# Performance work log

Measured on AMD Instinct MI355X. Metric: run time of the kernel, lower is better.

## Reference

```python
import jax, jax.numpy as jnp
import numpy as np

B, H, V, MSG_MAX_LEN = 16384, 512, 32, 20


def setup_inputs() -> dict:
    key = jax.random.key(0)
    ks = jax.random.split(key, 8)
    s = 0.05  # weight scale so softmax stays well-conditioned
    return {
        "encoder_hidden": jax.random.normal(ks[0], (B, H), jnp.float32),
        "encoder_cell": jax.random.normal(ks[1], (B, H), jnp.float32),
        "W_ih": jax.random.normal(ks[2], (4 * H, V), jnp.float32) * s,
        "b_ih": jax.random.normal(ks[3], (4 * H,), jnp.float32) * s,
        "W_hh": jax.random.normal(ks[4], (4 * H, H), jnp.float32) * s,
        "b_hh": jax.random.normal(ks[5], (4 * H,), jnp.float32) * s,
        "W_out": jax.random.normal(ks[6], (V, H), jnp.float32) * s,
        "b_out": jax.random.normal(ks[7], (V,), jnp.float32) * s,
        "init_input": jnp.zeros((1, V), jnp.float32),
        "eos_idx": 31,
    }


def reference(encoder_hidden, encoder_cell, W_ih, b_ih, W_hh, b_hh, W_out, b_out, init_input, eos_idx):
    batch = encoder_hidden.shape[0]
    vocab = W_out.shape[0]
    # Original code never updates decoder_input (typo 'deocder_input'), so the
    # LSTM input is init_input every step -> input projection is loop-invariant.
    x = jnp.broadcast_to(init_input, (batch, init_input.shape[1]))
    x_proj = x @ W_ih.T + b_ih  # [B, 4H]

    def step(carry, _):
        h, c, mask, lp = carry  # h,c: [B,H]; mask: [1,B]; lp: scalar
        mask_out = mask  # mask is appended BEFORE the update in the original
        gates = x_proj + h @ W_hh.T + b_hh
        i, f, g, o = jnp.split(gates, 4, axis=1)  # torch LSTMCell gate order i,f,g,o
        i = jax.nn.sigmoid(i); f = jax.nn.sigmoid(f)
        g = jnp.tanh(g); o = jax.nn.sigmoid(o)
        c = f * c + i * g
        h = o * jnp.tanh(c)
        probs = jax.nn.softmax(h @ W_out.T + b_out, axis=1)  # [B,V]
        predict = jax.nn.one_hot(jnp.argmax(probs, axis=1), vocab, dtype=probs.dtype)  # eval-mode branch
        lp = lp + jnp.log((probs * predict).sum(axis=1)) @ mask[0]
        new_mask = mask * (1.0 - predict[:, eos_idx])  # zero out finished sequences
        return (h, c, new_mask, lp), (predict, mask_out)

    init = (encoder_hidden, encoder_cell,
            jnp.ones((1, batch), encoder_hidden.dtype),
            jnp.zeros((), encoder_hidden.dtype))
    (_, _, _, log_probs), (message, mask) = jax.lax.scan(step, init, None, length=MSG_MAX_LEN)
    return message, mask, log_probs  # [L,B,V], [L,1,B], scalar
```

## Files before the change

kernel.cpp:

```cpp
#include <hip/hip_runtime.h>
#include <math.h>

#define BATCH 16384
#define HDIM  512
#define VOCAB 32
#define STEPS 20
#define G4    2048

typedef _Float16 f16;
typedef _Float16 f16x8 __attribute__((ext_vector_type(8)));
typedef float    f32x16 __attribute__((ext_vector_type(16)));

#define SH   256.0f
#define SW   1024.0f
#define SINV (1.0f / (SH * SW))


__device__ __forceinline__ void gload16(const void* g, void* l) {
#if defined(__has_builtin) && __has_builtin(__builtin_amdgcn_global_load_lds)
    __builtin_amdgcn_global_load_lds(
        (const __attribute__((address_space(1))) void*)g,
        (__attribute__((address_space(3))) void*)l, 16, 0, 0);
#else
    *(float4*)l = *(const float4*)g;
#endif
}

__device__ __forceinline__ float fsig(float x)  { return 1.0f / (1.0f + __expf(-x)); }
__device__ __forceinline__ float ftanh(float x) { return 1.0f - 2.0f / (__expf(2.0f * x) + 1.0f); }

__global__ void init_xb_kernel(const float* __restrict__ W_ih,
                               const float* __restrict__ b_ih,
                               const float* __restrict__ b_hh,
                               const float* __restrict__ x0,
                               float* __restrict__ xb) {
    int n = blockIdx.x * blockDim.x + threadIdx.x;
    if (n >= G4) return;
    float s = b_ih[n] + b_hh[n];
    const float* wr = W_ih + (size_t)n * VOCAB;
    #pragma unroll
    for (int v = 0; v < VOCAB; v++) s += wr[v] * x0[v];
    xb[n] = s;
}

__global__ void init_mask_kernel(float* __restrict__ mask) {
    int b = blockIdx.x * blockDim.x + threadIdx.x;
    if (b < BATCH) mask[b] = 1.0f;
}

__global__ void wimg_kernel(const float* __restrict__ W_hh,
                            f16* __restrict__ Wh, f16* __restrict__ Wl) {
    size_t g  = (size_t)blockIdx.x * 256 + threadIdx.x;
    int ln = g & 63;  size_t r = g >> 6;
    int gg = r & 3;   size_t r2 = r >> 2;
    int ks = r2 & 1;  size_t r3 = r2 >> 1;
    int kc = r3 & 15; int jb = (int)(r3 >> 4);
    int n = gg * 512 + jb * 32 + (ln & 31);
    int k = kc * 32 + ks * 16 + (ln >> 5) * 8;
    const float* s = W_hh + (size_t)n * HDIM + k;
    f16x8 vh, vl;
    #pragma unroll
    for (int i = 0; i < 8; i++) {
        float x = s[i] * SW;
        f16 h = (f16)x;
        vh[i] = h;
        vl[i] = (f16)(x - (float)h);
    }
    *(f16x8*)(Wh + g * 8) = vh;
    *(f16x8*)(Wl + g * 8) = vl;
}

__global__ void woutimg_kernel(const float* __restrict__ W_out,
                               f16* __restrict__ Oh, f16* __restrict__ Ol) {
    int g  = blockIdx.x * 256 + threadIdx.x;
    int ln = g & 63;
    int r  = g >> 6;
    int kc = r >> 1, ks = r & 1;
    int v  = ln & 31;
    int k  = kc * 32 + ks * 16 + (ln >> 5) * 8;
    const float* s = W_out + (size_t)v * HDIM + k;
    f16x8 vh, vl;
    #pragma unroll
    for (int i = 0; i < 8; i++) {
        float x = s[i] * SW;
        f16 h = (f16)x;
        vh[i] = h;
        vl[i] = (f16)(x - (float)h);
    }
    *(f16x8*)(Oh + (size_t)g * 8) = vh;
    *(f16x8*)(Ol + (size_t)g * 8) = vl;
}

__global__ void hT_init_kernel(const float* __restrict__ src,
                               f16* __restrict__ dh, f16* __restrict__ dl) {
    size_t g = (size_t)blockIdx.x * 256 + threadIdx.x;
    int ln = g & 63;  size_t r = g >> 6;
    int mb = (int)(r & 511); int kk = (int)(r >> 9);
    int m = mb * 32 + (ln & 31);
    int k = kk * 16 + (ln >> 5) * 8;
    const float* s = src + (size_t)m * HDIM + k;
    f16x8 vh, vl;
    #pragma unroll
    for (int i = 0; i < 8; i++) {
        float x = s[i] * SH;
        f16 h = (f16)x;
        vh[i] = h;
        vl[i] = (f16)(x - (float)h);
    }
    *(f16x8*)(dh + g * 8) = vh;
    *(f16x8*)(dl + g * 8) = vl;
}

__device__ __forceinline__ void out_body(int lane, int mb,
        const f16* __restrict__ hTh, const f16* __restrict__ hTl,
        const f16* __restrict__ Oh,  const f16* __restrict__ Ol,
        const float* __restrict__ b_out,
        float* __restrict__ mask, float* __restrict__ msg_t,
        float* __restrict__ maskout_t, float* __restrict__ lp_part, int eos) {
    const int half = lane >> 5;
    const int l31  = lane & 31;

    f32x16 acc;
    #pragma unroll
    for (int r = 0; r < 16; r++) acc[r] = 0.0f;

    f16x8 ah[3][2], al[3][2], bh[3][2], bl[3][2];
    auto load_frags = [&](int kc, int buf) {
        #pragma unroll
        for (int ks = 0; ks < 2; ks++) {
            size_t ga = ((size_t)(kc * 2 + ks) * 512 + mb) * 64 + lane;
            size_t gb = ((size_t)(kc * 2 + ks)) * 64 + lane;
            ah[buf][ks] = *(const f16x8*)(hTh + ga * 8);
            al[buf][ks] = *(const f16x8*)(hTl + ga * 8);
            bh[buf][ks] = *(const f16x8*)(Oh + gb * 8);
            bl[buf][ks] = *(const f16x8*)(Ol + gb * 8);
        }
    };

    load_frags(0, 0);
    load_frags(1, 1);
    for (int kc = 0; kc < 16; kc++) {
        if (kc < 14) load_frags(kc + 2, (kc + 2) % 3);
        int b = kc % 3;
        #pragma unroll
        for (int ks = 0; ks < 2; ks++) {
            acc = __builtin_amdgcn_mfma_f32_32x32x16_f16(ah[b][ks], bh[b][ks], acc, 0, 0, 0);
            acc = __builtin_amdgcn_mfma_f32_32x32x16_f16(ah[b][ks], bl[b][ks], acc, 0, 0, 0);
            acc = __builtin_amdgcn_mfma_f32_32x32x16_f16(al[b][ks], bh[b][ks], acc, 0, 0, 0);
        }
    }

    const float bo = b_out[l31];
    const int   m0 = mb * 32;
    float lpacc = 0.0f;

    #pragma unroll
    for (int reg = 0; reg < 16; reg++) {
        int row = (reg & 3) + 8 * (reg >> 2) + 4 * half;
        int m   = m0 + row;
        float logit = acc[reg] * SINV + bo;

        float mval = logit;
        int   midx = l31;
        #pragma unroll
        for (int off = 16; off > 0; off >>= 1) {
            float ov = __shfl_xor(mval, off, 32);
            int   oi = __shfl_xor(midx, off, 32);
            if (ov > mval || (ov == mval && oi < midx)) { mval = ov; midx = oi; }
        }
        float s = __expf(logit - mval);
        #pragma unroll
        for (int off = 16; off > 0; off >>= 1) s += __shfl_xor(s, off, 32);

        msg_t[(size_t)m * VOCAB + l31] = (l31 == midx) ? 1.0f : 0.0f;
        if (l31 == 0) {
            float mo = mask[m];
            maskout_t[m] = mo;
            lpacc += mo * (-__logf(s));
            if (midx == eos) mask[m] = 0.0f;
        }
    }
    lpacc += __shfl_xor(lpacc, 32);
    if (lane == 0) lp_part[mb] = lpacc;
}

__global__ __launch_bounds__(256, 2)
void step_fused(const f16* __restrict__ hT_h, const f16* __restrict__ hT_l,
                f16* __restrict__ hTo_h, f16* __restrict__ hTo_l,
                float* __restrict__ c,
                const f16* __restrict__ Wimg_h, const f16* __restrict__ Wimg_l,
                const float* __restrict__ xb,
                const f16* __restrict__ Oh, const f16* __restrict__ Ol,
                const float* __restrict__ b_out,
                float* __restrict__ mask,
                float* __restrict__ msg_p,
                float* __restrict__ maskout_p,
                float* __restrict__ lp_p,
                const int* __restrict__ eos_ptr,
                int has_out) {
    __shared__ __align__(16) char smem_raw[34048];
    f16* Blds = (f16*)smem_raw;

    const int tid  = threadIdx.x;
    const int lane = tid & 63;
    const int wave = tid >> 6;
    const int bid  = blockIdx.x;

    if (bid < 128) {
        if (!has_out) return;
        int mb = bid * 4 + wave;
        out_body(lane, mb, hT_h, hT_l, Oh, Ol, b_out,
                 mask, msg_p, maskout_p, lp_p, *eos_ptr);
        return;
    }

    const int gb   = bid - 128;
    const int wm   = wave;
    const int spw  = wave >> 1;
    const int ksw  = wave & 1;
    const int jb   = gb >> 6;
    const int mt64 = gb & 63;
    const int mb0  = mt64 * 8;
    const int m0   = mt64 * 256;
    const int j0   = jb * 32;
    const int half = lane >> 5;
    const int l31  = lane & 31;

    f32x16 acc[2][4];
    #pragma unroll
    for (int t = 0; t < 2; t++)
        #pragma unroll
        for (int g = 0; g < 4; g++)
            #pragma unroll
            for (int r = 0; r < 16; r++) acc[t][g][r] = 0.0f;

    const f16* bsrc0 = (spw ? Wimg_l : Wimg_h)
                     + ((size_t)jb * 128 + ksw * 4) * 512 + lane * 8;
    f16* bdst0 = Blds + (size_t)(spw * 8 + ksw * 4) * 512 + lane * 8;

    auto stage_b = [&](int kc, int buf) {
        const f16* s = bsrc0 + (size_t)kc * 4096;
        f16* d = bdst0 + buf * 16 * 512;
        #pragma unroll
        for (int g = 0; g < 4; g++)
            gload16(s + g * 512, d + g * 512);
    };

    const size_t abase0 = ((size_t)mb0 + wm * 2) * 512 + lane * 8;
    auto load_ah = [&](int kc, f16x8 (&dst)[2][2]) {
        #pragma unroll
        for (int ks = 0; ks < 2; ks++)
            #pragma unroll
            for (int t = 0; t < 2; t++)
                dst[ks][t] = *(const f16x8*)(hT_h + abase0
                               + (size_t)(kc * 2 + ks) * (512 * 512) + t * 512);
    };
    auto load_al = [&](int kc, f16x8 (&dst)[2][2]) {
        #pragma unroll
        for (int ks = 0; ks < 2; ks++)
            #pragma unroll
            for (int t = 0; t < 2; t++)
                dst[ks][t] = *(const f16x8*)(hT_l + abase0
                               + (size_t)(kc * 2 + ks) * (512 * 512) + t * 512);
    };

    auto compute = [&](f16x8 (&ah)[2][2], f16x8 (&al)[2][2], int buf) {
        #pragma unroll
        for (int ks = 0; ks < 2; ks++) {
            f16x8 bh[4], bl[4];
            #pragma unroll
            for (int g = 0; g < 4; g++) {
                bh[g] = *(const f16x8*)(Blds + (size_t)(buf * 16 + ks * 4 + g) * 512 + lane * 8);
                bl[g] = *(const f16x8*)(Blds + (size_t)(buf * 16 + 8 + ks * 4 + g) * 512 + lane * 8);
            }
            #pragma unroll
            for (int g = 0; g < 4; g++)
                #pragma unroll
                for (int t = 0; t < 2; t++)
                    acc[t][g] = __builtin_amdgcn_mfma_f32_32x32x16_f16(ah[ks][t], bh[g], acc[t][g], 0, 0, 0);
            #pragma unroll
            for (int g = 0; g < 4; g++)
                #pragma unroll
                for (int t = 0; t < 2; t++)
                    acc[t][g] = __builtin_amdgcn_mfma_f32_32x32x16_f16(ah[ks][t], bl[g], acc[t][g], 0, 0, 0);
            #pragma unroll
            for (int g = 0; g < 4; g++)
                #pragma unroll
                for (int t = 0; t < 2; t++)
                    acc[t][g] = __builtin_amdgcn_mfma_f32_32x32x16_f16(al[ks][t], bh[g], acc[t][g], 0, 0, 0);
        }
    };

    f16x8 ah0[2][2], ah1[2][2], al0[2][2], al1[2][2];
    stage_b(0, 0);
    load_ah(0, ah0);
    load_al(0, al0);
    for (int kc2 = 0; kc2 < 8; kc2++) {
        const int kc = kc2 * 2;
        __syncthreads();
        stage_b(kc + 1, 1);
        load_ah(kc + 1, ah1);
        load_al(kc + 1, al1);
        compute(ah0, al0, 0);
        __syncthreads();
        stage_b(kc + 2, 0);
        load_ah(kc + 2, ah0);
        load_al(kc + 2, al0);
        compute(ah1, al1, 1);
    }

    __syncthreads();
    unsigned int* hstage = (unsigned int*)smem_raw;

    const float xbi = xb[0 * HDIM + j0 + l31];
    const float xbf = xb[1 * HDIM + j0 + l31];
    const float xbg = xb[2 * HDIM + j0 + l31];
    const float xbo = xb[3 * HDIM + j0 + l31];
    #pragma unroll
    for (int t = 0; t < 2; t++) {
        #pragma unroll
        for (int reg = 0; reg < 16; reg++) {
            int row = (reg & 3) + 8 * (reg >> 2) + 4 * half;
            int ml  = wm * 64 + t * 32 + row;
            float gi = acc[t][0][reg] * SINV + xbi;
            float gf = acc[t][1][reg] * SINV + xbf;
            float gg = acc[t][2][reg] * SINV + xbg;
            float go = acc[t][3][reg] * SINV + xbo;
            float si = fsig(gi);
            float sf = fsig(gf);
            float tg = ftanh(gg);
            float so = fsig(go);
            size_t idx = (size_t)(m0 + ml) * HDIM + j0 + l31;
            float cn = sf * c[idx] + si * tg;
            c[idx] = cn;
            float hs = so * ftanh(cn) * SH;
            f16 hh = (f16)hs;
            f16 hl = (f16)(hs - (float)hh);
            union { f16 h[2]; unsigned int u; } pk;
            pk.h[0] = hh; pk.h[1] = hl;
            hstage[ml * 33 + l31] = pk.u;
        }
    }
    __syncthreads();

    #pragma unroll
    for (int s = 0; s < 4; s++) {
        int q   = tid + s * 256;
        int ksp = q >> 9;
        int mbl = (q >> 6) & 7;
        int ln  = q & 63;
        int mrow = mbl * 32 + (ln & 31);
        int jj8  = ksp * 16 + (ln >> 5) * 8;
        f16x8 vh, vl;
        #pragma unroll
        for (int i = 0; i < 8; i++) {
            union { unsigned int u; f16 h[2]; } pk;
            pk.u = hstage[mrow * 33 + jj8 + i];
            vh[i] = pk.h[0];
            vl[i] = pk.h[1];
        }
        size_t gq = ((size_t)(jb * 2 + ksp) * 512 + mb0 + mbl) * 64 + ln;
        *(f16x8*)(hTo_h + gq * 8) = vh;
        *(f16x8*)(hTo_l + gq * 8) = vl;
    }
}

__global__ __launch_bounds__(64)
void out_mfma(const f16* __restrict__ hTh, const f16* __restrict__ hTl,
              const f16* __restrict__ Oh, const f16* __restrict__ Ol,
              const float* __restrict__ b_out,
              float* __restrict__ mask,
              float* __restrict__ msg_t,
              float* __restrict__ maskout_t,
              float* __restrict__ lp_part,
              const int* __restrict__ eos_ptr) {
    out_body(threadIdx.x, blockIdx.x, hTh, hTl, Oh, Ol, b_out,
             mask, msg_t, maskout_t, lp_part, *eos_ptr);
}

__global__ void reduce_lp_kernel(const float* __restrict__ parts, int n,
                                 float* __restrict__ out) {
    __shared__ float sm[256];
    float s = 0.0f;
    for (int i = threadIdx.x; i < n; i += 256) s += parts[i];
    sm[threadIdx.x] = s;
    __syncthreads();
    for (int off = 128; off > 0; off >>= 1) {
        if (threadIdx.x < off) sm[threadIdx.x] += sm[threadIdx.x + off];
        __syncthreads();
    }
    if (threadIdx.x == 0) *out = sm[0];
}

extern "C" void kernel_launch(void* const* d_in, const int* in_sizes, int n_in,
                              void* d_out, int out_size, void* d_ws, size_t ws_size,
                              hipStream_t stream) {
    const float* enc_h  = (const float*)d_in[0];
    const float* enc_c  = (const float*)d_in[1];
    const float* W_ih   = (const float*)d_in[2];
    const float* b_ih   = (const float*)d_in[3];
    const float* W_hh   = (const float*)d_in[4];
    const float* b_hh   = (const float*)d_in[5];
    const float* W_out  = (const float*)d_in[6];
    const float* b_out  = (const float*)d_in[7];
    const float* x0     = (const float*)d_in[8];
    const int*   eosP   = (const int*)d_in[9];

    float* out     = (float*)d_out;
    float* msg     = out;
    float* maskout = out + (size_t)STEPS * BATCH * VOCAB;
    float* lp_out  = maskout + (size_t)STEPS * BATCH;

    const size_t NH = (size_t)BATCH * HDIM;
    char* w = (char*)d_ws;
    f16* hTh_a = (f16*)w;            w += NH * sizeof(f16);
    f16* hTl_a = (f16*)w;            w += NH * sizeof(f16);
    f16* hTh_b = (f16*)w;            w += NH * sizeof(f16);
    f16* hTl_b = (f16*)w;            w += NH * sizeof(f16);
    float* cbuf = (float*)w;         w += NH * sizeof(float);
    f16* Wimg_h = (f16*)w;           w += (size_t)G4 * HDIM * sizeof(f16);
    f16* Wimg_l = (f16*)w;           w += (size_t)G4 * HDIM * sizeof(f16);
    f16* Wout_h = (f16*)w;           w += (size_t)VOCAB * HDIM * sizeof(f16);
    f16* Wout_l = (f16*)w;           w += (size_t)VOCAB * HDIM * sizeof(f16);
    float* xb = (float*)w;           w += G4 * sizeof(float);
    float* maskbuf = (float*)w;      w += BATCH * sizeof(float);
    float* lp_parts = (float*)w;

    hipMemcpyAsync(cbuf, enc_c, NH * sizeof(float), hipMemcpyDeviceToDevice, stream);
    init_mask_kernel<<<(BATCH + 255) / 256, 256, 0, stream>>>(maskbuf);
    init_xb_kernel<<<(G4 + 255) / 256, 256, 0, stream>>>(W_ih, b_ih, b_hh, x0, xb);
    wimg_kernel<<<(G4 * HDIM / 8) / 256, 256, 0, stream>>>(W_hh, Wimg_h, Wimg_l);
    woutimg_kernel<<<8, 256, 0, stream>>>(W_out, Wout_h, Wout_l);
    hT_init_kernel<<<(int)((NH / 8) / 256), 256, 0, stream>>>(enc_h, hTh_a, hTl_a);

    for (int t = 0; t < STEPS; t++) {
        const f16* hi_in = (t & 1) ? hTh_b : hTh_a;
        const f16* lo_in = (t & 1) ? hTl_b : hTl_a;
        f16* hi_out      = (t & 1) ? hTh_a : hTh_b;
        f16* lo_out      = (t & 1) ? hTl_a : hTl_b;
        int tp = (t > 0) ? (t - 1) : 0;
        step_fused<<<1152, 256, 0, stream>>>(
            hi_in, lo_in, hi_out, lo_out, cbuf, Wimg_h, Wimg_l, xb,
            Wout_h, Wout_l, b_out, maskbuf,
            msg + (size_t)tp * BATCH * VOCAB,
            maskout + (size_t)tp * BATCH,
            lp_parts + (size_t)tp * 512,
            eosP, t > 0 ? 1 : 0);
    }
    {
        const f16* hi = (STEPS & 1) ? hTh_b : hTh_a;
        const f16* lo = (STEPS & 1) ? hTl_b : hTl_a;
        out_mfma<<<512, 64, 0, stream>>>(
            hi, lo, Wout_h, Wout_l, b_out, maskbuf,
            msg + (size_t)(STEPS - 1) * BATCH * VOCAB,
            maskout + (size_t)(STEPS - 1) * BATCH,
            lp_parts + (size_t)(STEPS - 1) * 512,
            eosP);
    }
    reduce_lp_kernel<<<1, 256, 0, stream>>>(lp_parts, STEPS * 512, lp_out);
}
```

Baseline: 2.498 ms.

## Halve per-block batch tile to 128 rows and raise occupancy to 3 blocks/CU

Shrinks the gate GEMM tile per block from 256 batch rows to 128 (one 32-row MFMA tile per wave instead of two), halving the accumulator registers, and doubles the grid to 2048 compute blocks. The block order is also changed so that the 16 column-blocks sharing a batch tile sit next to each other. Launch bounds now ask for 3 blocks per CU, aiming to hide more latency. The cost is that each W_hh tile staged in LDS is reused over half as many rows, so weight traffic from L2 roughly doubles.

New measurement: 2.492 ms. Within noise of the previous version (-0.3%).

```diff
diff --git a/kernel.cpp b/kernel.cpp
--- a/kernel.cpp
+++ b/kernel.cpp
@@ -184,7 +184,7 @@
     if (lane == 0) lp_part[mb] = lpacc;
 }
 
-__global__ __launch_bounds__(256, 2)
+__global__ __launch_bounds__(256, 3)
 void step_fused(const f16* __restrict__ hT_h, const f16* __restrict__ hT_l,
                 f16* __restrict__ hTo_h, f16* __restrict__ hTo_l,
                 float* __restrict__ c,
@@ -215,24 +215,21 @@
     }
 
     const int gb   = bid - 128;
-    const int wm   = wave;
+    const int jb   = gb & 15;
+    const int mt   = gb >> 4;
     const int spw  = wave >> 1;
     const int ksw  = wave & 1;
-    const int jb   = gb >> 6;
-    const int mt64 = gb & 63;
-    const int mb0  = mt64 * 8;
-    const int m0   = mt64 * 256;
+    const int mbA  = mt * 4 + wave;
+    const int m0   = mt * 128;
     const int j0   = jb * 32;
     const int half = lane >> 5;
     const int l31  = lane & 31;
 
-    f32x16 acc[2][4];
-    #pragma unroll
-    for (int t = 0; t < 2; t++)
-        #pragma unroll
-        for (int g = 0; g < 4; g++)
-            #pragma unroll
-            for (int r = 0; r < 16; r++) acc[t][g][r] = 0.0f;
+    f32x16 acc[4];
+    #pragma unroll
+    for (int g = 0; g < 4; g++)
+        #pragma unroll
+        for (int r = 0; r < 16; r++) acc[g][r] = 0.0f;
 
     const f16* bsrc0 = (spw ? Wimg_l : Wimg_h)
                      + ((size_t)jb * 128 + ksw * 4) * 512 + lane * 8;
@@ -246,25 +243,21 @@
             gload16(s + g * 512, d + g * 512);
     };
 
-    const size_t abase0 = ((size_t)mb0 + wm * 2) * 512 + lane * 8;
-    auto load_ah = [&](int kc, f16x8 (&dst)[2][2]) {
+    const size_t abase0 = (size_t)mbA * 512 + lane * 8;
+    auto load_ah = [&](int kc, f16x8 (&dst)[2]) {
         #pragma unroll
         for (int ks = 0; ks < 2; ks++)
-            #pragma unroll
-            for (int t = 0; t < 2; t++)
-                dst[ks][t] = *(const f16x8*)(hT_h + abase0
-                               + (size_t)(kc * 2 + ks) * (512 * 512) + t * 512);
+            dst[ks] = *(const f16x8*)(hT_h + abase0
+                           + (size_t)(kc * 2 + ks) * (512 * 512));
     };
-    auto load_al = [&](int kc, f16x8 (&dst)[2][2]) {
+    auto load_al = [&](int kc, f16x8 (&dst)[2]) {
         #pragma unroll
         for (int ks = 0; ks < 2; ks++)
-            #pragma unroll
-            for (int t = 0; t < 2; t++)
-                dst[ks][t] = *(const f16x8*)(hT_l + abase0
-                               + (size_t)(kc * 2 + ks) * (512 * 512) + t * 512);
+            dst[ks] = *(const f16x8*)(hT_l + abase0
+                           + (size_t)(kc * 2 + ks) * (512 * 512));
     };
 
-    auto compute = [&](f16x8 (&ah)[2][2], f16x8 (&al)[2][2], int buf) {
+    auto compute = [&](f16x8 (&ah)[2], f16x8 (&al)[2], int buf) {
         #pragma unroll
         for (int ks = 0; ks < 2; ks++) {
             f16x8 bh[4], bl[4];
@@ -275,23 +268,17 @@
             }
             #pragma unroll
             for (int g = 0; g < 4; g++)
-                #pragma unroll
-                for (int t = 0; t < 2; t++)
-                    acc[t][g] = __builtin_amdgcn_mfma_f32_32x32x16_f16(ah[ks][t], bh[g], acc[t][g], 0, 0, 0);
+                acc[g] = __builtin_amdgcn_mfma_f32_32x32x16_f16(ah[ks], bh[g], acc[g], 0, 0, 0);
             #pragma unroll
             for (int g = 0; g < 4; g++)
-                #pragma unroll
-                for (int t = 0; t < 2; t++)
-                    acc[t][g] = __builtin_amdgcn_mfma_f32_32x32x16_f16(ah[ks][t], bl[g], acc[t][g], 0, 0, 0);
+                acc[g] = __builtin_amdgcn_mfma_f32_32x32x16_f16(ah[ks], bl[g], acc[g], 0, 0, 0);
             #pragma unroll
             for (int g = 0; g < 4; g++)
-                #pragma unroll
-                for (int t = 0; t < 2; t++)
-                    acc[t][g] = __builtin_amdgcn_mfma_f32_32x32x16_f16(al[ks][t], bh[g], acc[t][g], 0, 0, 0);
+                acc[g] = __builtin_amdgcn_mfma_f32_32x32x16_f16(al[ks], bh[g], acc[g], 0, 0, 0);
         }
     };
 
-    f16x8 ah0[2][2], ah1[2][2], al0[2][2], al1[2][2];
+    f16x8 ah0[2], ah1[2], al0[2], al1[2];
     stage_b(0, 0);
     load_ah(0, ah0);
     load_al(0, al0);
@@ -317,37 +304,34 @@
     const float xbg = xb[2 * HDIM + j0 + l31];
     const float xbo = xb[3 * HDIM + j0 + l31];
     #pragma unroll
-    for (int t = 0; t < 2; t++) {
-        #pragma unroll
-        for (int reg = 0; reg < 16; reg++) {
-            int row = (reg & 3) + 8 * (reg >> 2) + 4 * half;
-            int ml  = wm * 64 + t * 32 + row;
-            float gi = acc[t][0][reg] * SINV + xbi;
-            float gf = acc[t][1][reg] * SINV + xbf;
-            float gg = acc[t][2][reg] * SINV + xbg;
-            float go = acc[t][3][reg] * SINV + xbo;
-            float si = fsig(gi);
-            float sf = fsig(gf);
-            float tg = ftanh(gg);
-            float so = fsig(go);
-            size_t idx = (size_t)(m0 + ml) * HDIM + j0 + l31;
-            float cn = sf * c[idx] + si * tg;
-            c[idx] = cn;
-            float hs = so * ftanh(cn) * SH;
-            f16 hh = (f16)hs;
-            f16 hl = (f16)(hs - (float)hh);
-            union { f16 h[2]; unsigned int u; } pk;
-            pk.h[0] = hh; pk.h[1] = hl;
-            hstage[ml * 33 + l31] = pk.u;
-        }
+    for (int reg = 0; reg < 16; reg++) {
+        int row = (reg & 3) + 8 * (reg >> 2) + 4 * half;
+        int ml  = wave * 32 + row;
+        float gi = acc[0][reg] * SINV + xbi;
+        float gf = acc[1][reg] * SINV + xbf;
+        float gg = acc[2][reg] * SINV + xbg;
+        float go = acc[3][reg] * SINV + xbo;
+        float si = fsig(gi);
+        float sf = fsig(gf);
+        float tg = ftanh(gg);
+        float so = fsig(go);
+        size_t idx = (size_t)(m0 + ml) * HDIM + j0 + l31;
+        float cn = sf * c[idx] + si * tg;
+        c[idx] = cn;
+        float hs = so * ftanh(cn) * SH;
+        f16 hh = (f16)hs;
+        f16 hl = (f16)(hs - (float)hh);
+        union { f16 h[2]; unsigned int u; } pk;
+        pk.h[0] = hh; pk.h[1] = hl;
+        hstage[ml * 33 + l31] = pk.u;
     }
     __syncthreads();
 
     #pragma unroll
-    for (int s = 0; s < 4; s++) {
+    for (int s = 0; s < 2; s++) {
         int q   = tid + s * 256;
-        int ksp = q >> 9;
-        int mbl = (q >> 6) & 7;
+        int ksp = q >> 8;
+        int mbl = (q >> 6) & 3;
         int ln  = q & 63;
         int mrow = mbl * 32 + (ln & 31);
         int jj8  = ksp * 16 + (ln >> 5) * 8;
@@ -359,7 +343,7 @@
             vh[i] = pk.h[0];
             vl[i] = pk.h[1];
         }
-        size_t gq = ((size_t)(jb * 2 + ksp) * 512 + mb0 + mbl) * 64 + ln;
+        size_t gq = ((size_t)(jb * 2 + ksp) * 512 + mt * 4 + mbl) * 64 + ln;
         *(f16x8*)(hTo_h + gq * 8) = vh;
         *(f16x8*)(hTo_l + gq * 8) = vl;
     }
@@ -439,7 +423,7 @@
         f16* hi_out      = (t & 1) ? hTh_a : hTh_b;
         f16* lo_out      = (t & 1) ? hTl_a : hTl_b;
         int tp = (t > 0) ? (t - 1) : 0;
-        step_fused<<<1152, 256, 0, stream>>>(
+        step_fused<<<2176, 256, 0, stream>>>(
             hi_in, lo_in, hi_out, lo_out, cbuf, Wimg_h, Wimg_l, xb,
             Wout_h, Wout_l, b_out, maskbuf,
             msg + (size_t)tp * BATCH * VOCAB,
```
